# Kernel optimization log

Hardware: AMD Instinct MI355X
Metric: run time of the kernel (lower is better)

Reference implementation:

```python
import math
import jax, jax.numpy as jnp
import numpy as np

ALPHA = 0.2                         # LeakyReLU slope
LAMBDA_INIT = 0.8 - 0.6 * math.exp(-0.3 * 1)  # lambda_init_fn(depth=1)
NEG_INF = -9e15
EPS_LN = 1e-5

B, N, IN_F, OUT_F = 4, 2048, 512, 512
INTERNAL = OUT_F // 2
REL_DIM = 10
NUM_REL = 6


def setup_inputs() -> dict:
    key = jax.random.key(0)
    ks = jax.random.split(key, 16)
    xav = lambda k, shape, fan: jax.random.normal(k, shape, jnp.float32) * (1.414 * math.sqrt(2.0 / fan))
    h = jax.random.normal(ks[0], (B, N, IN_F), jnp.float32)
    adj = jax.random.randint(ks[1], (B, N, N), 0, NUM_REL, jnp.int32)
    W = xav(ks[2], (IN_F, OUT_F), IN_F + OUT_F)
    a_left_pos = xav(ks[3], (INTERNAL,), INTERNAL + 1)
    a_right_pos = xav(ks[4], (INTERNAL,), INTERNAL + 1)
    a_left_neg = xav(ks[5], (INTERNAL,), INTERNAL + 1)
    a_right_neg = xav(ks[6], (INTERNAL,), INTERNAL + 1)
    rel_table = jax.random.normal(ks[7], (NUM_REL, REL_DIM), jnp.float32)
    a_rel_pos = xav(ks[8], (REL_DIM,), REL_DIM + 1)
    a_rel_neg = xav(ks[9], (REL_DIM,), REL_DIM + 1)
    ll1 = 0.1 * jax.random.normal(ks[10], (INTERNAL,), jnp.float32)
    lr1 = 0.1 * jax.random.normal(ks[11], (INTERNAL,), jnp.float32)
    ll2 = 0.1 * jax.random.normal(ks[12], (INTERNAL,), jnp.float32)
    lr2 = 0.1 * jax.random.normal(ks[13], (INTERNAL,), jnp.float32)
    ln_gamma = jnp.ones((OUT_F,), jnp.float32)
    ln_beta = jnp.zeros((OUT_F,), jnp.float32)
    return dict(h=h, adj=adj, W=W, a_left_pos=a_left_pos, a_right_pos=a_right_pos,
                a_left_neg=a_left_neg, a_right_neg=a_right_neg, rel_table=rel_table,
                a_rel_pos=a_rel_pos, a_rel_neg=a_rel_neg, ll1=ll1, lr1=lr1,
                ll2=ll2, lr2=lr2, ln_gamma=ln_gamma, ln_beta=ln_beta)


def _leaky(x):
    return jnp.where(x >= 0, x, ALPHA * x)


def reference(h, adj, W, a_left_pos, a_right_pos, a_left_neg, a_right_neg,
              rel_table, a_rel_pos, a_rel_neg, ll1, lr1, ll2, lr2,
              ln_gamma, ln_beta):
    # Projection: Wh [B,N,out] -> split into pos/neg halves [B,N,internal]
    Wh = jnp.einsum('bni,io->bno', h, W)
    Bn, Nn, _ = Wh.shape
    Wh2 = Wh.reshape(Bn, Nn, 2, INTERNAL)
    Wh_pos, Wh_neg = Wh2[:, :, 0, :], Wh2[:, :, 1, :]

    # Additive GAT-style scores: e[b,i,j] = a_left.Wh[i] + a_right.Wh[j]
    e_pos = (Wh_pos @ a_left_pos)[:, :, None] + (Wh_pos @ a_right_pos)[:, None, :]
    e_neg = (Wh_neg @ a_left_neg)[:, :, None] + (Wh_neg @ a_right_neg)[:, None, :]

    # Relation-embedding bias: gather [B,N,N,rel_dim] then project to scalar
    rel_emb = rel_table[adj]                       # [B,N,N,R]
    e_pos = e_pos + rel_emb @ a_rel_pos
    e_neg = e_neg + rel_emb @ a_rel_neg

    mask = adj > 0
    att_pos = jax.nn.softmax(jnp.where(mask, _leaky(e_pos), NEG_INF), axis=2)
    att_neg = jax.nn.softmax(jnp.where(mask, _leaky(e_neg), NEG_INF), axis=2)

    lam = jnp.exp(jnp.sum(ll1 * lr1)) - jnp.exp(jnp.sum(ll2 * lr2)) + LAMBDA_INIT
    attention = att_pos - lam * att_neg            # dropout is identity (eval)

    Wh_v = jnp.concatenate([Wh_pos, Wh_neg], axis=-1)   # [B,N,out]
    h_prime = jnp.einsum('bij,bjd->bid', attention, Wh_v)

    mu = jnp.mean(h_prime, axis=-1, keepdims=True)
    var = jnp.mean(jnp.square(h_prime - mu), axis=-1, keepdims=True)
    h_prime = (h_prime - mu) / jnp.sqrt(var + EPS_LN) * ln_gamma + ln_beta
    h_prime = h_prime * (1 - LAMBDA_INIT)
    return jax.nn.gelu(h_prime, approximate=False), attention
```

## Files before the change

### kernel.cpp

```cpp
#include <hip/hip_runtime.h>
#include <hip/hip_bf16.h>


#define B_ 4
#define N_ 2048
#define F_ 512
#define ALPHA_ 0.2f
#define NEG_INF_ -9000000000000000.0f
#define EPS_LN_ 1e-5f

typedef __attribute__((ext_vector_type(8))) short bf16x8;
typedef __attribute__((ext_vector_type(4))) float f32x4;

#define HBF_OFF   0
#define WHT_OFF   0
#define WT_OFF    8388608
#define WH_OFF    8912896
#define HP_OFF    8912896
#define ATTBF_OFF 25690112
#define EL_OFF    59244544
#define SC_OFF    59375616
#define FLAG_OFF  59375680
#define CANON_OFF 59375744

#define C_ALP 0
#define C_ARP 256
#define C_ALN 512
#define C_ARN 768
#define C_GAM 2128
#define C_BET 2640

__device__ __forceinline__ float bf_as_f32(unsigned short u) {
    return __uint_as_float(((unsigned)u) << 16);
}
__device__ __forceinline__ float ldf(const void* p, long i, int isf32) {
    return isf32 ? ((const float*)p)[i] : bf_as_f32(((const unsigned short*)p)[i]);
}
__device__ __forceinline__ short f2bf(float f) {
    __hip_bfloat16 t = __float2bfloat16(f);
    return *reinterpret_cast<short*>(&t);
}

#define GLL16(g, l) __builtin_amdgcn_global_load_lds( \
    (const __attribute__((address_space(1))) void*)(g), \
    (__attribute__((address_space(3))) void*)(l), 16, 0, 0)

__global__ void k_prep(const unsigned short* __restrict__ hraw,
                       const void* alp, const void* arp, const void* aln, const void* arn,
                       const void* rel, const void* arelp, const void* areln,
                       const void* ll1, const void* lr1, const void* ll2, const void* lr2,
                       const void* gam, const void* bet,
                       int* __restrict__ flag, float* __restrict__ canon, float* __restrict__ sc) {
    __shared__ float wmax[4];
    __shared__ int s_fl;
    int tid = threadIdx.x, lane = tid & 63, wid = tid >> 6;
    float mx = 0.f;
    for (int i = tid; i < 8192; i += 256) {
        float v = fabsf(bf_as_f32(hraw[i]));
        if (v == v && v > mx) mx = v;
    }
    for (int off = 32; off; off >>= 1) mx = fmaxf(mx, __shfl_down(mx, off));
    if (lane == 0) wmax[wid] = mx;
    __syncthreads();
    if (tid == 0) {
        float m = fmaxf(fmaxf(wmax[0], wmax[1]), fmaxf(wmax[2], wmax[3]));
        int f = (m > 1e10f) ? 1 : 0;
        s_fl = f; flag[0] = f;
    }
    __syncthreads();
    int fl = s_fl;
    canon[C_ALP + tid] = ldf(alp, tid, fl);
    canon[C_ARP + tid] = ldf(arp, tid, fl);
    canon[C_ALN + tid] = ldf(aln, tid, fl);
    canon[C_ARN + tid] = ldf(arn, tid, fl);
    canon[C_GAM + tid] = ldf(gam, tid, fl);
    canon[C_GAM + 256 + tid] = ldf(gam, 256 + tid, fl);
    canon[C_BET + tid] = ldf(bet, tid, fl);
    canon[C_BET + 256 + tid] = ldf(bet, 256 + tid, fl);
    if (wid == 0) {
        float s1 = 0.f, s2 = 0.f;
        for (int k = lane; k < 256; k += 64) {
            s1 += ldf(ll1, k, fl) * ldf(lr1, k, fl);
            s2 += ldf(ll2, k, fl) * ldf(lr2, k, fl);
        }
        for (int off = 32; off; off >>= 1) { s1 += __shfl_down(s1, off); s2 += __shfl_down(s2, off); }
        if (lane == 0) {
            float lam_init = 0.8f - 0.6f * expf(-0.3f);
            sc[0] = expf(s1) - expf(s2) + lam_init;
        }
    } else if (wid == 1 && lane < 6) {
        float p = 0.f, n = 0.f;
        for (int d = 0; d < 10; ++d) {
            float rv = ldf(rel, lane * 10 + d, fl);
            p += rv * ldf(arelp, d, fl);
            n += rv * ldf(areln, d, fl);
        }
        sc[1 + lane] = p;
        sc[7 + lane] = n;
    }
}

__global__ __launch_bounds__(256) void k_conv_h8(const void* __restrict__ h, const int* __restrict__ flag,
                                                 short* __restrict__ hbf) {
    int fl = flag[0];
    int i = (blockIdx.x * 256 + threadIdx.x) * 8;
    bf16x8 v;
    if (fl) {
        const float4* p = (const float4*)((const float*)h + i);
        float4 a = p[0], b = p[1];
        v[0] = f2bf(a.x); v[1] = f2bf(a.y); v[2] = f2bf(a.z); v[3] = f2bf(a.w);
        v[4] = f2bf(b.x); v[5] = f2bf(b.y); v[6] = f2bf(b.z); v[7] = f2bf(b.w);
    } else {
        v = *(const bf16x8*)((const short*)h + i);
    }
    *(bf16x8*)(hbf + i) = v;
}

__global__ __launch_bounds__(256) void k_transW(const void* __restrict__ W, const int* __restrict__ flag,
                                                __hip_bfloat16* __restrict__ Wt) {
    __shared__ float t[32][33];
    int fl = flag[0];
    int k0 = blockIdx.x * 32, o0 = blockIdx.y * 32;
    int tx = threadIdx.x & 31, ty = threadIdx.x >> 5;
#pragma unroll
    for (int r = 0; r < 4; ++r)
        t[ty + r * 8][tx] = ldf(W, (k0 + ty + r * 8) * 512 + o0 + tx, fl);
    __syncthreads();
#pragma unroll
    for (int r = 0; r < 4; ++r)
        Wt[(o0 + ty + r * 8) * 512 + k0 + tx] = __float2bfloat16(t[tx][ty + r * 8]);
}

__global__ __launch_bounds__(256) void k_gemm128(const short* __restrict__ A, const short* __restrict__ B,
                                                 float* __restrict__ C, int K, int N,
                                                 long aBatch, long bBatch, long cBatch) {
    __shared__ short As[128 * 32];
    __shared__ short Bs[128 * 32];
    int tid = threadIdx.x, wid = tid >> 6, lane = tid & 63;
    int bm = blockIdx.x * 128, bn = blockIdx.y * 128;
    int bz = blockIdx.z;
    const short* Ab = A + bz * aBatch + (long)bm * K;
    const short* Bb = B + bz * bBatch + (long)bn * K;
    f32x4 acc[4][4] = {};
    int wr = (wid >> 1) * 64, wc = (wid & 1) * 64;
    int c0 = wid * 64 + lane, c1 = c0 + 256;
    int r0 = c0 >> 2, q0 = (c0 & 3) * 8;
    int r1 = c1 >> 2, q1 = (c1 & 3) * 8;
    int l15 = lane & 15, kh = (lane >> 4) * 8;
    for (int k0 = 0; k0 < K; k0 += 32) {
        __syncthreads();
        GLL16(Ab + (long)r0 * K + k0 + q0, As + c0 * 8);
        GLL16(Ab + (long)r1 * K + k0 + q1, As + c1 * 8);
        GLL16(Bb + (long)r0 * K + k0 + q0, Bs + c0 * 8);
        GLL16(Bb + (long)r1 * K + k0 + q1, Bs + c1 * 8);
        __syncthreads();
        bf16x8 af[4], bq[4];
#pragma unroll
        for (int m = 0; m < 4; ++m) af[m] = *(const bf16x8*)&As[(wr + m * 16 + l15) * 32 + kh];
#pragma unroll
        for (int n = 0; n < 4; ++n) bq[n] = *(const bf16x8*)&Bs[(wc + n * 16 + l15) * 32 + kh];
#pragma unroll
        for (int m = 0; m < 4; ++m)
#pragma unroll
            for (int n = 0; n < 4; ++n)
                acc[m][n] = __builtin_amdgcn_mfma_f32_16x16x32_bf16(af[m], bq[n], acc[m][n], 0, 0, 0);
    }
    int rg = (lane >> 4) * 4;
#pragma unroll
    for (int m = 0; m < 4; ++m)
#pragma unroll
        for (int n = 0; n < 4; ++n)
#pragma unroll
            for (int r = 0; r < 4; ++r) {
                int row = bm + wr + m * 16 + rg + r;
                int col = bn + wc + n * 16 + l15;
                C[bz * cBatch + (long)row * N + col] = acc[m][n][r];
            }
}

__global__ __launch_bounds__(256) void k_transWh(const float* __restrict__ Wh, __hip_bfloat16* __restrict__ Wht) {
    __shared__ float t[32][33];
    int b = blockIdx.z;
    int o0 = blockIdx.x * 32, j0 = blockIdx.y * 32;
    int tx = threadIdx.x & 31, ty = threadIdx.x >> 5;
#pragma unroll
    for (int r = 0; r < 4; ++r)
        t[ty + r * 8][tx] = Wh[(b * 2048 + j0 + ty + r * 8) * 512 + o0 + tx];
    __syncthreads();
#pragma unroll
    for (int r = 0; r < 4; ++r)
        Wht[((long)b * 512 + o0 + ty + r * 8) * 2048 + j0 + tx] = __float2bfloat16(t[tx][ty + r * 8]);
}

__global__ __launch_bounds__(256) void k_edots(const float* __restrict__ Wh, const float* __restrict__ canon,
                                               float* __restrict__ el) {
    int wid = threadIdx.x >> 6, lane = threadIdx.x & 63;
    int m = blockIdx.x * 4 + wid;
    float selp = 0.f, serp = 0.f, seln = 0.f, sern = 0.f;
#pragma unroll
    for (int t = 0; t < 4; ++t) {
        int k = t * 64 + lane;
        float wp = Wh[m * 512 + k];
        float wn = Wh[m * 512 + 256 + k];
        selp += wp * canon[C_ALP + k];
        serp += wp * canon[C_ARP + k];
        seln += wn * canon[C_ALN + k];
        sern += wn * canon[C_ARN + k];
    }
    for (int off = 32; off; off >>= 1) {
        selp += __shfl_down(selp, off); serp += __shfl_down(serp, off);
        seln += __shfl_down(seln, off); sern += __shfl_down(sern, off);
    }
    if (lane == 0) {
        el[m] = selp; el[8192 + m] = serp; el[16384 + m] = seln; el[24576 + m] = sern;
    }
}

__global__ __launch_bounds__(256) void k_attn(const int* __restrict__ adj,
                                              const float* __restrict__ el, const float* __restrict__ sc,
                                              float* __restrict__ att_f32,
                                              __hip_bfloat16* __restrict__ att_bf) {
    __shared__ float s_rp[6], s_rn[6], s_lam[1];
    __shared__ float rmp[4], rmn[4], rsp[4], rsn[4];
    int tid = threadIdx.x, lane = tid & 63, wid = tid >> 6;
    if (tid < 6) { s_rp[tid] = sc[1 + tid]; s_rn[tid] = sc[7 + tid]; }
    if (tid == 6) s_lam[0] = sc[0];
    int m = blockIdx.x, b = m >> 11;
    float elp = el[m], eln = el[16384 + m];
    const float* erp = el + 8192 + b * 2048;
    const float* ern = el + 24576 + b * 2048;
    const int* adjr = adj + (long)m * 2048;
    __syncthreads();
    float sp[8], sn[8];
    float mp = NEG_INF_, mn = NEG_INF_;
#pragma unroll
    for (int t = 0; t < 8; ++t) {
        int j = t * 256 + tid;
        int a = adjr[j];
        float ep = elp + erp[j] + s_rp[a];
        float en = eln + ern[j] + s_rn[a];
        ep = ep >= 0.f ? ep : ALPHA_ * ep;
        en = en >= 0.f ? en : ALPHA_ * en;
        sp[t] = a > 0 ? ep : NEG_INF_;
        sn[t] = a > 0 ? en : NEG_INF_;
        mp = fmaxf(mp, sp[t]); mn = fmaxf(mn, sn[t]);
    }
    for (int off = 32; off; off >>= 1) { mp = fmaxf(mp, __shfl_down(mp, off)); mn = fmaxf(mn, __shfl_down(mn, off)); }
    if (lane == 0) { rmp[wid] = mp; rmn[wid] = mn; }
    __syncthreads();
    mp = fmaxf(fmaxf(rmp[0], rmp[1]), fmaxf(rmp[2], rmp[3]));
    mn = fmaxf(fmaxf(rmn[0], rmn[1]), fmaxf(rmn[2], rmn[3]));
    float sump = 0.f, sumn = 0.f;
#pragma unroll
    for (int t = 0; t < 8; ++t) {
        sp[t] = __expf(sp[t] - mp);
        sn[t] = __expf(sn[t] - mn);
        sump += sp[t]; sumn += sn[t];
    }
    for (int off = 32; off; off >>= 1) { sump += __shfl_down(sump, off); sumn += __shfl_down(sumn, off); }
    if (lane == 0) { rsp[wid] = sump; rsn[wid] = sumn; }
    __syncthreads();
    sump = rsp[0] + rsp[1] + rsp[2] + rsp[3];
    sumn = rsn[0] + rsn[1] + rsn[2] + rsn[3];
    float ip = 1.0f / sump, inn = 1.0f / sumn;
    float lam = s_lam[0];
#pragma unroll
    for (int t = 0; t < 8; ++t) {
        float v = sp[t] * ip - lam * sn[t] * inn;
        long idx = (long)m * 2048 + t * 256 + tid;
        att_f32[idx] = v;
        att_bf[idx] = __float2bfloat16(v);
    }
}

__global__ __launch_bounds__(256) void k_lngelu(const float* __restrict__ HP, const float* __restrict__ canon,
                                                float* __restrict__ out) {
    int wid = threadIdx.x >> 6, lane = threadIdx.x & 63;
    int m = blockIdx.x * 4 + wid;
    float x[8]; float s = 0.f, ss = 0.f;
#pragma unroll
    for (int t = 0; t < 8; ++t) {
        x[t] = HP[m * 512 + t * 64 + lane];
        s += x[t]; ss += x[t] * x[t];
    }
    for (int off = 32; off; off >>= 1) { s += __shfl_xor(s, off); ss += __shfl_xor(ss, off); }
    float mu = s * (1.0f / 512.0f);
    float var = ss * (1.0f / 512.0f) - mu * mu;
    float inv = rsqrtf(fmaxf(var, 0.0f) + EPS_LN_);
    float scale = 1.0f - (0.8f - 0.6f * expf(-0.3f));
#pragma unroll
    for (int t = 0; t < 8; ++t) {
        int k = t * 64 + lane;
        float y = (x[t] - mu) * inv * canon[C_GAM + k] + canon[C_BET + k];
        y *= scale;
        float g = 0.5f * y * (1.0f + erff(y * 0.70710678118654752f));
        out[m * 512 + k] = g;
    }
}

extern "C" void kernel_launch(void* const* d_in, const int* in_sizes, int n_in,
                              void* d_out, int out_size, void* d_ws, size_t ws_size,
                              hipStream_t stream) {
    const void* h   = d_in[0];
    const int*  adj = (const int*)d_in[1];
    const void* W   = d_in[2];

    char* ws = (char*)d_ws;
    short*          hbf   = (short*)(ws + HBF_OFF);
    __hip_bfloat16* Wt    = (__hip_bfloat16*)(ws + WT_OFF);
    float*          Wh    = (float*)(ws + WH_OFF);
    __hip_bfloat16* Wht   = (__hip_bfloat16*)(ws + WHT_OFF);
    __hip_bfloat16* attbf = (__hip_bfloat16*)(ws + ATTBF_OFF);
    float*          el    = (float*)(ws + EL_OFF);
    float*          sc    = (float*)(ws + SC_OFF);
    int*            flg   = (int*)(ws + FLAG_OFF);
    float*          can   = (float*)(ws + CANON_OFF);
    float*          HP    = (float*)(ws + HP_OFF);

    float* out_gelu = (float*)d_out;
    float* out_att  = out_gelu + (size_t)B_ * N_ * F_;

    k_prep<<<1, 256, 0, stream>>>((const unsigned short*)h,
                                  d_in[3], d_in[4], d_in[5], d_in[6], d_in[7], d_in[8], d_in[9],
                                  d_in[10], d_in[11], d_in[12], d_in[13], d_in[14], d_in[15],
                                  flg, can, sc);
    k_conv_h8<<<2048, 256, 0, stream>>>(h, flg, hbf);
    k_transW<<<dim3(16, 16), 256, 0, stream>>>(W, flg, Wt);
    k_gemm128<<<dim3(64, 4, 1), 256, 0, stream>>>(hbf, (const short*)Wt, Wh, 512, 512, 0, 0, 0);
    k_transWh<<<dim3(16, 64, 4), 256, 0, stream>>>(Wh, Wht);
    k_edots<<<2048, 256, 0, stream>>>(Wh, can, el);
    k_attn<<<8192, 256, 0, stream>>>(adj, el, sc, out_att, attbf);
    k_gemm128<<<dim3(16, 4, 4), 256, 0, stream>>>((const short*)attbf, (const short*)Wht, HP, 2048, 512,
                                                  2048L * 2048, 512L * 2048, 2048L * 512);
    k_lngelu<<<2048, 256, 0, stream>>>(HP, can, out_gelu);
}
```

Baseline: 287.7 us.

## Fuse projection transpose into GEMM epilogue and precompute edge dots via W·a

Folds the attention-vector dot products into W (v = W·a computed in the W transpose with atomics), so the edge scores come straight from h in the conversion kernel, and the separate edots kernel goes away. The first GEMM now writes transposed bf16 Wh directly through an LDS epilogue, which removes the fp32 Wh buffer and the transpose kernel. The GEMM moves to a 128x64 tile with K-step 64 and an XOR-swizzled LDS layout. Attention, softmax and LN/GELU loads and stores are vectorised. The trade-offs are extra atomics and a slightly different rounding order for the edge scores, since they are computed from h rather than from rounded Wh.

```diff
diff --git a/kernel.cpp b/kernel.cpp
--- a/kernel.cpp
+++ b/kernel.cpp
@@ -10,18 +10,19 @@
 #define EPS_LN_ 1e-5f
 
 typedef __attribute__((ext_vector_type(8))) short bf16x8;
+typedef __attribute__((ext_vector_type(4))) short bf16x4;
 typedef __attribute__((ext_vector_type(4))) float f32x4;
 
 #define HBF_OFF   0
-#define WHT_OFF   0
 #define WT_OFF    8388608
-#define WH_OFF    8912896
-#define HP_OFF    8912896
-#define ATTBF_OFF 25690112
-#define EL_OFF    59244544
-#define SC_OFF    59375616
-#define FLAG_OFF  59375680
-#define CANON_OFF 59375744
+#define EL_OFF    8912896
+#define HP_OFF    0
+#define WHT_OFF   16777216
+#define ATTBF_OFF 25165824
+#define CANON_OFF 58720256
+#define SC_OFF    58732864
+#define FLAG_OFF  58732928
+#define V_OFF     58736640
 
 #define C_ALP 0
 #define C_ARP 256
@@ -50,14 +51,15 @@
                        const void* rel, const void* arelp, const void* areln,
                        const void* ll1, const void* lr1, const void* ll2, const void* lr2,
                        const void* gam, const void* bet,
-                       int* __restrict__ flag, float* __restrict__ canon, float* __restrict__ sc) {
+                       int* __restrict__ flag, float* __restrict__ canon, float* __restrict__ sc,
+                       float* __restrict__ v) {
     __shared__ float wmax[4];
     __shared__ int s_fl;
     int tid = threadIdx.x, lane = tid & 63, wid = tid >> 6;
     float mx = 0.f;
     for (int i = tid; i < 8192; i += 256) {
-        float v = fabsf(bf_as_f32(hraw[i]));
-        if (v == v && v > mx) mx = v;
+        float x = fabsf(bf_as_f32(hraw[i]));
+        if (x == x && x > mx) mx = x;
     }
     for (int off = 32; off; off >>= 1) mx = fmaxf(mx, __shfl_down(mx, off));
     if (lane == 0) wmax[wid] = mx;
@@ -69,6 +71,7 @@
     }
     __syncthreads();
     int fl = s_fl;
+    for (int i = tid; i < 2048; i += 256) v[i] = 0.f;
     canon[C_ALP + tid] = ldf(alp, tid, fl);
     canon[C_ARP + tid] = ldf(arp, tid, fl);
     canon[C_ALN + tid] = ldf(aln, tid, fl);
@@ -100,24 +103,9 @@
     }
 }
 
-__global__ __launch_bounds__(256) void k_conv_h8(const void* __restrict__ h, const int* __restrict__ flag,
-                                                 short* __restrict__ hbf) {
-    int fl = flag[0];
-    int i = (blockIdx.x * 256 + threadIdx.x) * 8;
-    bf16x8 v;
-    if (fl) {
-        const float4* p = (const float4*)((const float*)h + i);
-        float4 a = p[0], b = p[1];
-        v[0] = f2bf(a.x); v[1] = f2bf(a.y); v[2] = f2bf(a.z); v[3] = f2bf(a.w);
-        v[4] = f2bf(b.x); v[5] = f2bf(b.y); v[6] = f2bf(b.z); v[7] = f2bf(b.w);
-    } else {
-        v = *(const bf16x8*)((const short*)h + i);
-    }
-    *(bf16x8*)(hbf + i) = v;
-}
-
 __global__ __launch_bounds__(256) void k_transW(const void* __restrict__ W, const int* __restrict__ flag,
-                                                __hip_bfloat16* __restrict__ Wt) {
+                                                __hip_bfloat16* __restrict__ Wt,
+                                                const float* __restrict__ canon, float* __restrict__ v) {
     __shared__ float t[32][33];
     int fl = flag[0];
     int k0 = blockIdx.x * 32, o0 = blockIdx.y * 32;
@@ -129,90 +117,150 @@
 #pragma unroll
     for (int r = 0; r < 4; ++r)
         Wt[(o0 + ty + r * 8) * 512 + k0 + tx] = __float2bfloat16(t[tx][ty + r * 8]);
-}
-
-__global__ __launch_bounds__(256) void k_gemm128(const short* __restrict__ A, const short* __restrict__ B,
-                                                 float* __restrict__ C, int K, int N,
-                                                 long aBatch, long bBatch, long cBatch) {
-    __shared__ short As[128 * 32];
-    __shared__ short Bs[128 * 32];
+    int kl = threadIdx.x >> 3;
+    int seg = threadIdx.x & 7;
+    int neg = o0 >= 256;
+    const float* aL = canon + (neg ? C_ALN : C_ALP) + (o0 & 255);
+    const float* aR = canon + (neg ? C_ARN : C_ARP) + (o0 & 255);
+    float s0 = 0.f, s1 = 0.f;
+#pragma unroll
+    for (int e = 0; e < 4; ++e) {
+        float w = t[kl][seg * 4 + e];
+        s0 += w * aL[seg * 4 + e];
+        s1 += w * aR[seg * 4 + e];
+    }
+    s0 += __shfl_xor(s0, 1); s0 += __shfl_xor(s0, 2); s0 += __shfl_xor(s0, 4);
+    s1 += __shfl_xor(s1, 1); s1 += __shfl_xor(s1, 2); s1 += __shfl_xor(s1, 4);
+    if (seg == 0) {
+        int vb = neg ? 2 : 0;
+        atomicAdd(&v[(vb + 0) * 512 + k0 + kl], s0);
+        atomicAdd(&v[(vb + 1) * 512 + k0 + kl], s1);
+    }
+}
+
+__global__ __launch_bounds__(256) void k_conv_h8(const void* __restrict__ h, const int* __restrict__ flag,
+                                                 short* __restrict__ hbf, const float* __restrict__ v,
+                                                 float* __restrict__ el) {
+    int fl = flag[0];
+    int tid = threadIdx.x, lane = tid & 63;
+    long i = ((long)blockIdx.x * 256 + tid) * 8;
+    int row = (int)(i >> 9);
+    float f[8];
+    if (fl) {
+        const float4* p = (const float4*)((const float*)h + i);
+        float4 a = p[0], b = p[1];
+        f[0] = a.x; f[1] = a.y; f[2] = a.z; f[3] = a.w;
+        f[4] = b.x; f[5] = b.y; f[6] = b.z; f[7] = b.w;
+    } else {
+        bf16x8 x = *(const bf16x8*)((const short*)h + i);
+#pragma unroll
+        for (int e = 0; e < 8; ++e) f[e] = bf_as_f32((unsigned short)x[e]);
+    }
+    bf16x8 vv;
+#pragma unroll
+    for (int e = 0; e < 8; ++e) vv[e] = f2bf(f[e]);
+    *(bf16x8*)(hbf + i) = vv;
+    const float* v0 = v + 0 * 512 + lane * 8;
+    const float* v1 = v + 1 * 512 + lane * 8;
+    const float* v2 = v + 2 * 512 + lane * 8;
+    const float* v3 = v + 3 * 512 + lane * 8;
+    float slp = 0.f, srp = 0.f, sln = 0.f, srn = 0.f;
+#pragma unroll
+    for (int e = 0; e < 8; ++e) {
+        slp += f[e] * v0[e]; srp += f[e] * v1[e];
+        sln += f[e] * v2[e]; srn += f[e] * v3[e];
+    }
+    for (int off = 32; off; off >>= 1) {
+        slp += __shfl_xor(slp, off); srp += __shfl_xor(srp, off);
+        sln += __shfl_xor(sln, off); srn += __shfl_xor(srn, off);
+    }
+    if (lane == 0) {
+        el[row] = slp; el[8192 + row] = srp; el[16384 + row] = sln; el[24576 + row] = srn;
+    }
+}
+
+template<int TRANS_OUT>
+__global__ __launch_bounds__(256) void k_gemm(const short* __restrict__ A, const short* __restrict__ B,
+                                              void* __restrict__ Cout, int K, int N,
+                                              long aBatch, long bBatch, long cBatch) {
+    __shared__ short SM[12288];
+    short* As = SM;
+    short* Bs = SM + 8192;
     int tid = threadIdx.x, wid = tid >> 6, lane = tid & 63;
-    int bm = blockIdx.x * 128, bn = blockIdx.y * 128;
-    int bz = blockIdx.z;
+    int bm = blockIdx.x * 128, bn = blockIdx.y * 64, bz = blockIdx.z;
     const short* Ab = A + bz * aBatch + (long)bm * K;
     const short* Bb = B + bz * bBatch + (long)bn * K;
-    f32x4 acc[4][4] = {};
-    int wr = (wid >> 1) * 64, wc = (wid & 1) * 64;
-    int c0 = wid * 64 + lane, c1 = c0 + 256;
-    int r0 = c0 >> 2, q0 = (c0 & 3) * 8;
-    int r1 = c1 >> 2, q1 = (c1 & 3) * 8;
-    int l15 = lane & 15, kh = (lane >> 4) * 8;
-    for (int k0 = 0; k0 < K; k0 += 32) {
+    f32x4 acc[4][2] = {};
+    int wr = (wid >> 1) * 64, wc = (wid & 1) * 32;
+    int l15 = lane & 15, lhi = lane >> 4;
+    for (int k0 = 0; k0 < K; k0 += 64) {
         __syncthreads();
-        GLL16(Ab + (long)r0 * K + k0 + q0, As + c0 * 8);
-        GLL16(Ab + (long)r1 * K + k0 + q1, As + c1 * 8);
-        GLL16(Bb + (long)r0 * K + k0 + q0, Bs + c0 * 8);
-        GLL16(Bb + (long)r1 * K + k0 + q1, Bs + c1 * 8);
+#pragma unroll
+        for (int j = 0; j < 4; ++j) {
+            int q = tid + j * 256;
+            int row = q >> 3, c = (q & 7) ^ (row & 7);
+            GLL16(Ab + (long)row * K + k0 + c * 8, As + q * 8);
+        }
+#pragma unroll
+        for (int j = 0; j < 2; ++j) {
+            int q = tid + j * 256;
+            int row = q >> 3, c = (q & 7) ^ (row & 7);
+            GLL16(Bb + (long)row * K + k0 + c * 8, Bs + q * 8);
+        }
         __syncthreads();
-        bf16x8 af[4], bq[4];
-#pragma unroll
-        for (int m = 0; m < 4; ++m) af[m] = *(const bf16x8*)&As[(wr + m * 16 + l15) * 32 + kh];
-#pragma unroll
-        for (int n = 0; n < 4; ++n) bq[n] = *(const bf16x8*)&Bs[(wc + n * 16 + l15) * 32 + kh];
+#pragma unroll
+        for (int ks = 0; ks < 2; ++ks) {
+            bf16x8 af[4], bq[2];
+#pragma unroll
+            for (int m = 0; m < 4; ++m) {
+                int r = wr + m * 16 + l15;
+                int c = (ks * 4 + lhi) ^ (r & 7);
+                af[m] = *(const bf16x8*)&As[r * 64 + c * 8];
+            }
+#pragma unroll
+            for (int n = 0; n < 2; ++n) {
+                int r = wc + n * 16 + l15;
+                int c = (ks * 4 + lhi) ^ (r & 7);
+                bq[n] = *(const bf16x8*)&Bs[r * 64 + c * 8];
+            }
+#pragma unroll
+            for (int m = 0; m < 4; ++m)
+#pragma unroll
+                for (int n = 0; n < 2; ++n)
+                    acc[m][n] = __builtin_amdgcn_mfma_f32_16x16x32_bf16(af[m], bq[n], acc[m][n], 0, 0, 0);
+        }
+    }
+    int rg = lhi * 4;
+    if (TRANS_OUT == 0) {
+        float* C = (float*)Cout + bz * cBatch;
 #pragma unroll
         for (int m = 0; m < 4; ++m)
 #pragma unroll
-            for (int n = 0; n < 4; ++n)
-                acc[m][n] = __builtin_amdgcn_mfma_f32_16x16x32_bf16(af[m], bq[n], acc[m][n], 0, 0, 0);
-    }
-    int rg = (lane >> 4) * 4;
-#pragma unroll
-    for (int m = 0; m < 4; ++m)
-#pragma unroll
-        for (int n = 0; n < 4; ++n)
-#pragma unroll
-            for (int r = 0; r < 4; ++r) {
-                int row = bm + wr + m * 16 + rg + r;
-                int col = bn + wc + n * 16 + l15;
-                C[bz * cBatch + (long)row * N + col] = acc[m][n][r];
+            for (int n = 0; n < 2; ++n)
+#pragma unroll
+                for (int r = 0; r < 4; ++r)
+                    C[(long)(bm + wr + m * 16 + rg + r) * N + bn + wc + n * 16 + l15] = acc[m][n][r];
+    } else {
+        __syncthreads();
+        short* T = SM;
+#pragma unroll
+        for (int m = 0; m < 4; ++m)
+#pragma unroll
+            for (int n = 0; n < 2; ++n) {
+                bf16x4 p;
+#pragma unroll
+                for (int r = 0; r < 4; ++r) p[r] = f2bf(acc[m][n][r]);
+                int o = wc + n * 16 + l15;
+                int jj = wr + m * 16 + rg;
+                *(bf16x4*)&T[o * 136 + jj] = p;
             }
-}
-
-__global__ __launch_bounds__(256) void k_transWh(const float* __restrict__ Wh, __hip_bfloat16* __restrict__ Wht) {
-    __shared__ float t[32][33];
-    int b = blockIdx.z;
-    int o0 = blockIdx.x * 32, j0 = blockIdx.y * 32;
-    int tx = threadIdx.x & 31, ty = threadIdx.x >> 5;
-#pragma unroll
-    for (int r = 0; r < 4; ++r)
-        t[ty + r * 8][tx] = Wh[(b * 2048 + j0 + ty + r * 8) * 512 + o0 + tx];
-    __syncthreads();
-#pragma unroll
-    for (int r = 0; r < 4; ++r)
-        Wht[((long)b * 512 + o0 + ty + r * 8) * 2048 + j0 + tx] = __float2bfloat16(t[tx][ty + r * 8]);
-}
-
-__global__ __launch_bounds__(256) void k_edots(const float* __restrict__ Wh, const float* __restrict__ canon,
-                                               float* __restrict__ el) {
-    int wid = threadIdx.x >> 6, lane = threadIdx.x & 63;
-    int m = blockIdx.x * 4 + wid;
-    float selp = 0.f, serp = 0.f, seln = 0.f, sern = 0.f;
-#pragma unroll
-    for (int t = 0; t < 4; ++t) {
-        int k = t * 64 + lane;
-        float wp = Wh[m * 512 + k];
-        float wn = Wh[m * 512 + 256 + k];
-        selp += wp * canon[C_ALP + k];
-        serp += wp * canon[C_ARP + k];
-        seln += wn * canon[C_ALN + k];
-        sern += wn * canon[C_ARN + k];
-    }
-    for (int off = 32; off; off >>= 1) {
-        selp += __shfl_down(selp, off); serp += __shfl_down(serp, off);
-        seln += __shfl_down(seln, off); sern += __shfl_down(sern, off);
-    }
-    if (lane == 0) {
-        el[m] = selp; el[8192 + m] = serp; el[16384 + m] = seln; el[24576 + m] = sern;
+        __syncthreads();
+        int b = bm >> 11, jb = bm & 2047;
+        int o = tid >> 2, sg = tid & 3;
+        short* Wg = (short*)Cout + ((long)b * 512 + bn + o) * 2048 + jb + sg * 32;
+#pragma unroll
+        for (int w2 = 0; w2 < 4; ++w2)
+            *(bf16x8*)(Wg + w2 * 8) = *(bf16x8*)&T[o * 136 + sg * 32 + w2 * 8];
     }
 }
 
@@ -220,7 +268,7 @@
                                               const float* __restrict__ el, const float* __restrict__ sc,
                                               float* __restrict__ att_f32,
                                               __hip_bfloat16* __restrict__ att_bf) {
-    __shared__ float s_rp[6], s_rn[6], s_lam[1];
+    __shared__ float s_rp[8], s_rn[8], s_lam[1];
     __shared__ float rmp[4], rmn[4], rsp[4], rsn[4];
     int tid = threadIdx.x, lane = tid & 63, wid = tid >> 6;
     if (tid < 6) { s_rp[tid] = sc[1 + tid]; s_rn[tid] = sc[7 + tid]; }
@@ -231,19 +279,25 @@
     const float* ern = el + 24576 + b * 2048;
     const int* adjr = adj + (long)m * 2048;
     __syncthreads();
+    int j0 = tid * 8;
+    int4 A0 = *(const int4*)(adjr + j0), A1 = *(const int4*)(adjr + j0 + 4);
+    float4 P0 = *(const float4*)(erp + j0), P1 = *(const float4*)(erp + j0 + 4);
+    float4 Q0 = *(const float4*)(ern + j0), Q1 = *(const float4*)(ern + j0 + 4);
+    int aa[8] = {A0.x, A0.y, A0.z, A0.w, A1.x, A1.y, A1.z, A1.w};
+    float rp[8] = {P0.x, P0.y, P0.z, P0.w, P1.x, P1.y, P1.z, P1.w};
+    float rn[8] = {Q0.x, Q0.y, Q0.z, Q0.w, Q1.x, Q1.y, Q1.z, Q1.w};
     float sp[8], sn[8];
     float mp = NEG_INF_, mn = NEG_INF_;
 #pragma unroll
-    for (int t = 0; t < 8; ++t) {
-        int j = t * 256 + tid;
-        int a = adjr[j];
-        float ep = elp + erp[j] + s_rp[a];
-        float en = eln + ern[j] + s_rn[a];
+    for (int e = 0; e < 8; ++e) {
+        int a = aa[e];
+        float ep = elp + rp[e] + s_rp[a];
+        float en = eln + rn[e] + s_rn[a];
         ep = ep >= 0.f ? ep : ALPHA_ * ep;
         en = en >= 0.f ? en : ALPHA_ * en;
-        sp[t] = a > 0 ? ep : NEG_INF_;
-        sn[t] = a > 0 ? en : NEG_INF_;
-        mp = fmaxf(mp, sp[t]); mn = fmaxf(mn, sn[t]);
+        sp[e] = a > 0 ? ep : NEG_INF_;
+        sn[e] = a > 0 ? en : NEG_INF_;
+        mp = fmaxf(mp, sp[e]); mn = fmaxf(mn, sn[e]);
     }
     for (int off = 32; off; off >>= 1) { mp = fmaxf(mp, __shfl_down(mp, off)); mn = fmaxf(mn, __shfl_down(mn, off)); }
     if (lane == 0) { rmp[wid] = mp; rmn[wid] = mn; }
@@ -252,10 +306,10 @@
     mn = fmaxf(fmaxf(rmn[0], rmn[1]), fmaxf(rmn[2], rmn[3]));
     float sump = 0.f, sumn = 0.f;
 #pragma unroll
-    for (int t = 0; t < 8; ++t) {
-        sp[t] = __expf(sp[t] - mp);
-        sn[t] = __expf(sn[t] - mn);
-        sump += sp[t]; sumn += sn[t];
+    for (int e = 0; e < 8; ++e) {
+        sp[e] = __expf(sp[e] - mp);
+        sn[e] = __expf(sn[e] - mn);
+        sump += sp[e]; sumn += sn[e];
     }
     for (int off = 32; off; off >>= 1) { sump += __shfl_down(sump, off); sumn += __shfl_down(sumn, off); }
     if (lane == 0) { rsp[wid] = sump; rsn[wid] = sumn; }
@@ -264,38 +318,46 @@
     sumn = rsn[0] + rsn[1] + rsn[2] + rsn[3];
     float ip = 1.0f / sump, inn = 1.0f / sumn;
     float lam = s_lam[0];
-#pragma unroll
-    for (int t = 0; t < 8; ++t) {
-        float v = sp[t] * ip - lam * sn[t] * inn;
-        long idx = (long)m * 2048 + t * 256 + tid;
-        att_f32[idx] = v;
-        att_bf[idx] = __float2bfloat16(v);
-    }
+    float vout[8];
+    bf16x8 vb;
+#pragma unroll
+    for (int e = 0; e < 8; ++e) {
+        vout[e] = sp[e] * ip - lam * sn[e] * inn;
+        vb[e] = f2bf(vout[e]);
+    }
+    float* of = att_f32 + (long)m * 2048 + j0;
+    *(float4*)(of)     = make_float4(vout[0], vout[1], vout[2], vout[3]);
+    *(float4*)(of + 4) = make_float4(vout[4], vout[5], vout[6], vout[7]);
+    *(bf16x8*)((short*)att_bf + (long)m * 2048 + j0) = vb;
 }
 
 __global__ __launch_bounds__(256) void k_lngelu(const float* __restrict__ HP, const float* __restrict__ canon,
                                                 float* __restrict__ out) {
     int wid = threadIdx.x >> 6, lane = threadIdx.x & 63;
     int m = blockIdx.x * 4 + wid;
-    float x[8]; float s = 0.f, ss = 0.f;
-#pragma unroll
-    for (int t = 0; t < 8; ++t) {
-        x[t] = HP[m * 512 + t * 64 + lane];
-        s += x[t]; ss += x[t] * x[t];
-    }
+    const float* Hr = HP + (long)m * 512 + lane * 8;
+    float4 x0 = *(const float4*)(Hr), x1 = *(const float4*)(Hr + 4);
+    float x[8] = {x0.x, x0.y, x0.z, x0.w, x1.x, x1.y, x1.z, x1.w};
+    float s = 0.f, ss = 0.f;
+#pragma unroll
+    for (int e = 0; e < 8; ++e) { s += x[e]; ss += x[e] * x[e]; }
     for (int off = 32; off; off >>= 1) { s += __shfl_xor(s, off); ss += __shfl_xor(ss, off); }
     float mu = s * (1.0f / 512.0f);
     float var = ss * (1.0f / 512.0f) - mu * mu;
     float inv = rsqrtf(fmaxf(var, 0.0f) + EPS_LN_);
     float scale = 1.0f - (0.8f - 0.6f * expf(-0.3f));
-#pragma unroll
-    for (int t = 0; t < 8; ++t) {
-        int k = t * 64 + lane;
-        float y = (x[t] - mu) * inv * canon[C_GAM + k] + canon[C_BET + k];
+    const float* g8 = canon + C_GAM + lane * 8;
+    const float* b8 = canon + C_BET + lane * 8;
+    float o[8];
+#pragma unroll
+    for (int e = 0; e < 8; ++e) {
+        float y = (x[e] - mu) * inv * g8[e] + b8[e];
         y *= scale;
-        float g = 0.5f * y * (1.0f + erff(y * 0.70710678118654752f));
-        out[m * 512 + k] = g;
-    }
+        o[e] = 0.5f * y * (1.0f + erff(y * 0.70710678118654752f));
+    }
+    float* op = out + (long)m * 512 + lane * 8;
+    *(float4*)(op)     = make_float4(o[0], o[1], o[2], o[3]);
+    *(float4*)(op + 4) = make_float4(o[4], o[5], o[6], o[7]);
 }
 
 extern "C" void kernel_launch(void* const* d_in, const int* in_sizes, int n_in,
@@ -308,14 +370,14 @@
     char* ws = (char*)d_ws;
     short*          hbf   = (short*)(ws + HBF_OFF);
     __hip_bfloat16* Wt    = (__hip_bfloat16*)(ws + WT_OFF);
-    float*          Wh    = (float*)(ws + WH_OFF);
+    float*          el    = (float*)(ws + EL_OFF);
+    float*          HP    = (float*)(ws + HP_OFF);
     __hip_bfloat16* Wht   = (__hip_bfloat16*)(ws + WHT_OFF);
     __hip_bfloat16* attbf = (__hip_bfloat16*)(ws + ATTBF_OFF);
-    float*          el    = (float*)(ws + EL_OFF);
+    float*          can   = (float*)(ws + CANON_OFF);
     float*          sc    = (float*)(ws + SC_OFF);
     int*            flg   = (int*)(ws + FLAG_OFF);
-    float*          can   = (float*)(ws + CANON_OFF);
-    float*          HP    = (float*)(ws + HP_OFF);
+    float*          v     = (float*)(ws + V_OFF);
 
     float* out_gelu = (float*)d_out;
     float* out_att  = out_gelu + (size_t)B_ * N_ * F_;
@@ -323,14 +385,12 @@
     k_prep<<<1, 256, 0, stream>>>((const unsigned short*)h,
                                   d_in[3], d_in[4], d_in[5], d_in[6], d_in[7], d_in[8], d_in[9],
                                   d_in[10], d_in[11], d_in[12], d_in[13], d_in[14], d_in[15],
-                                  flg, can, sc);
-    k_conv_h8<<<2048, 256, 0, stream>>>(h, flg, hbf);
-    k_transW<<<dim3(16, 16), 256, 0, stream>>>(W, flg, Wt);
-    k_gemm128<<<dim3(64, 4, 1), 256, 0, stream>>>(hbf, (const short*)Wt, Wh, 512, 512, 0, 0, 0);
-    k_transWh<<<dim3(16, 64, 4), 256, 0, stream>>>(Wh, Wht);
-    k_edots<<<2048, 256, 0, stream>>>(Wh, can, el);
+                                  flg, can, sc, v);
+    k_transW<<<dim3(16, 16), 256, 0, stream>>>(W, flg, Wt, can, v);
+    k_conv_h8<<<2048, 256, 0, stream>>>(h, flg, hbf, v, el);
+    k_gemm<1><<<dim3(64, 8, 1), 256, 0, stream>>>(hbf, (const short*)Wt, Wht, 512, 512, 0, 0, 0);
     k_attn<<<8192, 256, 0, stream>>>(adj, el, sc, out_att, attbf);
-    k_gemm128<<<dim3(16, 4, 4), 256, 0, stream>>>((const short*)attbf, (const short*)Wht, HP, 2048, 512,
+    k_gemm<0><<<dim3(16, 8, 4), 256, 0, stream>>>((const short*)attbf, (const short*)Wht, HP, 2048, 512,
                                                   2048L * 2048, 512L * 2048, 2048L * 512);
     k_lngelu<<<2048, 256, 0, stream>>>(HP, can, out_gelu);
 }
```

New measurement: 276.2 us. -4.0%, faster.
